# Kernel tuning notes

Hardware: AMD Instinct MI355X
Metric: run time of the kernel (lower is better)

The kernel has to match this reference:

```python
import jax, jax.numpy as jnp
import numpy as np

B, H, W, C = 32, 64, 64, 256


def setup_inputs() -> dict:
    key = jax.random.key(0)
    kq, kk, kv = jax.random.split(key, 3)
    query = jax.random.normal(kq, (B, H, W, C), dtype=jnp.float32)
    keys = jax.random.normal(kk, (B, H, W, C), dtype=jnp.float32)
    values = jax.random.normal(kv, (B, H, W, C), dtype=jnp.float32)
    return {"query": query, "keys": keys, "values": values}


def reference(query, keys, values):
    # A[b,q,k] = sum_{h,w} query[b,h,w,q] * keys[b,h,w,k]
    scores = jnp.einsum("bhwq,bhwk->bqk", query, keys)
    attn = jax.nn.softmax(scores, axis=-1)  # softmax over keys axis
    # out[b,q,h,w] = sum_k attn[b,q,k] * values[b,h,w,k]
    out = jnp.einsum("bqk,bhwk->bqhw", attn, values)
    return out
```

## Files before the change

### kernel.cpp

```cpp
#include <hip/hip_runtime.h>
#include <hip/hip_bf16.h>

#define B_  32
#define HW_ 4096
#define C_  256
#define S_LDS 40

using bf16x8 = __attribute__((ext_vector_type(8))) short;
using f32x4  = __attribute__((ext_vector_type(4))) float;

__device__ __forceinline__ ushort f2bf_rn(float x) {
    uint u = __builtin_bit_cast(uint, x);
    u += 0x7FFFu + ((u >> 16) & 1u);
    return (ushort)(u >> 16);
}
__device__ __forceinline__ uint pk_bf2(float a, float b) {
    return ((uint)f2bf_rn(b) << 16) | (uint)f2bf_rn(a);
}
__device__ __forceinline__ uint pk_rtz(float x0, float x1) {
    return __builtin_amdgcn_perm(__builtin_bit_cast(uint, x1),
                                 __builtin_bit_cast(uint, x0), 0x07060302u);
}
__device__ __forceinline__ void split2_rtz(float x0, float x1, uint& hi2, uint& lo2) {
    uint u0 = __builtin_bit_cast(uint, x0), u1 = __builtin_bit_cast(uint, x1);
    hi2 = __builtin_amdgcn_perm(u1, u0, 0x07060302u);
    float h0 = __builtin_bit_cast(float, u0 & 0xFFFF0000u);
    float h1 = __builtin_bit_cast(float, u1 & 0xFFFF0000u);
    lo2 = pk_rtz(x0 - h0, x1 - h1);
}

__global__ __launch_bounds__(256) void scores_kernel(const float* __restrict__ qg,
                                                     const float* __restrict__ kg,
                                                     float* __restrict__ scores) {
    int x  = blockIdx.x;
    int s  = x & 3;
    int tn = (x >> 2) & 3;
    int tm = (x >> 4) & 1;
    int b  = x >> 5;

    __shared__ __align__(16) ushort Qhi[128 * S_LDS], Qlo[128 * S_LDS];
    __shared__ __align__(16) ushort Khi[64 * S_LDS],  Klo[64 * S_LDS];

    int tid = threadIdx.x, lane = tid & 63, w = tid >> 6;
    int m0 = (w >> 1) * 64;
    int n0 = (w & 1) * 32;
    int g = lane >> 4, r16 = lane & 15;

    int cq = tid & 127;
    int hq = (tid >> 7) * 16;
    int ck = tid & 63;
    int hk = (tid >> 6) * 8;

    const float* qcol = qg + (size_t)b * HW_ * C_ + tm * 128 + cq;
    const float* kcol = kg + (size_t)b * HW_ * C_ + tn * 64 + ck;

    f32x4 acc[4][2];
#pragma unroll
    for (int i = 0; i < 4; ++i)
#pragma unroll
        for (int j = 0; j < 2; ++j) acc[i][j] = (f32x4){0.f, 0.f, 0.f, 0.f};

#define LOAD_QK(qr, kr, itv) {                                                 \
        int hw0 = s * 1024 + (itv) * 32;                                       \
        const float* qp = qcol + (size_t)(hw0 + hq) * C_;                      \
        _Pragma("unroll")                                                      \
        for (int j = 0; j < 16; ++j) qr[j] = qp[(size_t)j * C_];               \
        const float* kp = kcol + (size_t)(hw0 + hk) * C_;                      \
        _Pragma("unroll")                                                      \
        for (int j = 0; j < 8; ++j) kr[j] = kp[(size_t)j * C_];                \
    }

#define CONVERT_STORE(qr, kr) {                                                \
        uint qh[8], ql[8];                                                     \
        _Pragma("unroll")                                                      \
        for (int p = 0; p < 8; ++p) split2_rtz(qr[2*p], qr[2*p+1], qh[p], ql[p]); \
        int qb_ = cq * S_LDS + hq;                                             \
        *reinterpret_cast<uint4*>(&Qhi[qb_])     = make_uint4(qh[0], qh[1], qh[2], qh[3]); \
        *reinterpret_cast<uint4*>(&Qhi[qb_ + 8]) = make_uint4(qh[4], qh[5], qh[6], qh[7]); \
        *reinterpret_cast<uint4*>(&Qlo[qb_])     = make_uint4(ql[0], ql[1], ql[2], ql[3]); \
        *reinterpret_cast<uint4*>(&Qlo[qb_ + 8]) = make_uint4(ql[4], ql[5], ql[6], ql[7]); \
        uint kh[4], kl[4];                                                     \
        _Pragma("unroll")                                                      \
        for (int p = 0; p < 4; ++p) split2_rtz(kr[2*p], kr[2*p+1], kh[p], kl[p]); \
        int kb_ = ck * S_LDS + hk;                                             \
        *reinterpret_cast<uint4*>(&Khi[kb_]) = make_uint4(kh[0], kh[1], kh[2], kh[3]); \
        *reinterpret_cast<uint4*>(&Klo[kb_]) = make_uint4(kl[0], kl[1], kl[2], kl[3]); \
    }

#define MFMA_PHASE() {                                                         \
        bf16x8 ahi[4], alo[4];                                                 \
        _Pragma("unroll")                                                      \
        for (int mi = 0; mi < 4; ++mi) {                                       \
            int off = (m0 + mi * 16 + r16) * S_LDS + g * 8;                    \
            ahi[mi] = *reinterpret_cast<const bf16x8*>(&Qhi[off]);             \
            alo[mi] = *reinterpret_cast<const bf16x8*>(&Qlo[off]);             \
        }                                                                      \
        _Pragma("unroll")                                                      \
        for (int ni = 0; ni < 2; ++ni) {                                       \
            int off = (n0 + ni * 16 + r16) * S_LDS + g * 8;                    \
            bf16x8 bhi = *reinterpret_cast<const bf16x8*>(&Khi[off]);          \
            bf16x8 blo = *reinterpret_cast<const bf16x8*>(&Klo[off]);          \
            _Pragma("unroll")                                                  \
            for (int mi = 0; mi < 4; ++mi) {                                   \
                acc[mi][ni] = __builtin_amdgcn_mfma_f32_16x16x32_bf16(ahi[mi], bhi, acc[mi][ni], 0, 0, 0); \
                acc[mi][ni] = __builtin_amdgcn_mfma_f32_16x16x32_bf16(ahi[mi], blo, acc[mi][ni], 0, 0, 0); \
                acc[mi][ni] = __builtin_amdgcn_mfma_f32_16x16x32_bf16(alo[mi], bhi, acc[mi][ni], 0, 0, 0); \
            }                                                                  \
        }                                                                      \
    }

#define STEP(qc, kc, qn, kn, itv, doload) {                                    \
        if (doload) LOAD_QK(qn, kn, (itv) + 1);                                \
        __syncthreads();                                                       \
        CONVERT_STORE(qc, kc);                                                 \
        __syncthreads();                                                       \
        MFMA_PHASE();                                                          \
    }

    float qa[16], ka[8], qb[16], kb[8];
    LOAD_QK(qa, ka, 0);
    for (int p = 0; p < 16; ++p) {
        STEP(qa, ka, qb, kb, 2 * p, true);
        STEP(qb, kb, qa, ka, 2 * p + 1, p < 15);
    }

#pragma unroll
    for (int mi = 0; mi < 4; ++mi)
#pragma unroll
        for (int ni = 0; ni < 2; ++ni)
#pragma unroll
            for (int r = 0; r < 4; ++r) {
                int qrow = tm * 128 + m0 + mi * 16 + g * 4 + r;
                int kc   = tn * 64 + n0 + ni * 16 + r16;
                atomicAdd(&scores[((size_t)b * 256 + qrow) * 256 + kc], acc[mi][ni][r]);
            }
#undef STEP
#undef MFMA_PHASE
#undef CONVERT_STORE
#undef LOAD_QK
}

__global__ __launch_bounds__(256) void softmax_kernel(const float* __restrict__ scores,
                                                      ushort* __restrict__ attn) {
    int wid  = blockIdx.x * 4 + (threadIdx.x >> 6);
    int lane = threadIdx.x & 63;
    const float4 v = *reinterpret_cast<const float4*>(scores + (size_t)wid * 256 + lane * 4);
    float m = fmaxf(fmaxf(v.x, v.y), fmaxf(v.z, v.w));
#pragma unroll
    for (int off = 32; off; off >>= 1) m = fmaxf(m, __shfl_xor(m, off, 64));
    float e0 = __expf(v.x - m), e1 = __expf(v.y - m), e2 = __expf(v.z - m), e3 = __expf(v.w - m);
    float ssum = e0 + e1 + e2 + e3;
#pragma unroll
    for (int off = 32; off; off >>= 1) ssum += __shfl_xor(ssum, off, 64);
    float inv = 1.0f / ssum;
    uint2 o;
    o.x = pk_bf2(e0 * inv, e1 * inv);
    o.y = pk_bf2(e2 * inv, e3 * inv);
    *reinterpret_cast<uint2*>(attn + (size_t)wid * 256 + lane * 4) = o;
}

__global__ __launch_bounds__(256) void pv_kernel(const ushort* __restrict__ attn,
                                                 const float* __restrict__ vg,
                                                 float* __restrict__ out) {
    int b   = blockIdx.x >> 6;
    int hw0 = (blockIdx.x & 63) * 64;
    int tid = threadIdx.x, lane = tid & 63, w = tid >> 6;
    int m0  = w * 64;
    int g   = lane >> 4, r16 = lane & 15;

    f32x4 acc[4][4];
#pragma unroll
    for (int i = 0; i < 4; ++i)
#pragma unroll
        for (int j = 0; j < 4; ++j) acc[i][j] = (f32x4){0.f, 0.f, 0.f, 0.f};

    for (int ks = 0; ks < 8; ++ks) {
        int k0 = ks * 32;
        bf16x8 a[4];
#pragma unroll
        for (int mi = 0; mi < 4; ++mi) {
            int qrow = m0 + mi * 16 + r16;
            a[mi] = *reinterpret_cast<const bf16x8*>(attn + ((size_t)b * 256 + qrow) * 256 + k0 + g * 8);
        }
        float4 vv[4][2];
#pragma unroll
        for (int ni = 0; ni < 4; ++ni) {
            int hw = hw0 + ni * 16 + r16;
            const float* vp = vg + ((size_t)(b * HW_ + hw)) * C_ + k0 + g * 8;
            vv[ni][0] = *reinterpret_cast<const float4*>(vp);
            vv[ni][1] = *reinterpret_cast<const float4*>(vp + 4);
        }
#pragma unroll
        for (int ni = 0; ni < 4; ++ni) {
            bf16x8 bf;
            uint* bu = reinterpret_cast<uint*>(&bf);
            bu[0] = pk_rtz(vv[ni][0].x, vv[ni][0].y);
            bu[1] = pk_rtz(vv[ni][0].z, vv[ni][0].w);
            bu[2] = pk_rtz(vv[ni][1].x, vv[ni][1].y);
            bu[3] = pk_rtz(vv[ni][1].z, vv[ni][1].w);
#pragma unroll
            for (int mi = 0; mi < 4; ++mi)
                acc[mi][ni] = __builtin_amdgcn_mfma_f32_16x16x32_bf16(a[mi], bf, acc[mi][ni], 0, 0, 0);
        }
    }

#pragma unroll
    for (int mi = 0; mi < 4; ++mi)
#pragma unroll
        for (int ni = 0; ni < 4; ++ni)
#pragma unroll
            for (int r = 0; r < 4; ++r) {
                int qrow = m0 + mi * 16 + g * 4 + r;
                int hw   = hw0 + ni * 16 + r16;
                out[((size_t)b * 256 + qrow) * 4096 + hw] = acc[mi][ni][r];
            }
}

extern "C" void kernel_launch(void* const* d_in, const int* in_sizes, int n_in,
                              void* d_out, int out_size, void* d_ws, size_t ws_size,
                              hipStream_t stream) {
    const float* q = (const float*)d_in[0];
    const float* k = (const float*)d_in[1];
    const float* v = (const float*)d_in[2];
    float* out = (float*)d_out;

    float*  scores = (float*)d_ws;
    ushort* attn   = (ushort*)((char*)d_ws + (size_t)B_ * 256 * 256 * 4);

    (void)hipMemsetAsync(d_ws, 0, (size_t)B_ * 256 * 256 * 4, stream);
    scores_kernel<<<1024, 256, 0, stream>>>(q, k, scores);
    softmax_kernel<<<2048, 256, 0, stream>>>(scores, attn);
    pv_kernel<<<2048, 256, 0, stream>>>(attn, v, out);
}
```

Baseline: 215.3 us.

## Enlarge scores tile to 128x128 per block and double-buffer PV loads

```diff
diff --git a/kernel.cpp b/kernel.cpp
--- a/kernel.cpp
+++ b/kernel.cpp
@@ -29,30 +29,28 @@
     lo2 = pk_rtz(x0 - h0, x1 - h1);
 }
 
-__global__ __launch_bounds__(256) void scores_kernel(const float* __restrict__ qg,
-                                                     const float* __restrict__ kg,
-                                                     float* __restrict__ scores) {
+__global__ __launch_bounds__(512, 4) void scores_kernel(const float* __restrict__ qg,
+                                                        const float* __restrict__ kg,
+                                                        float* __restrict__ scores) {
     int x  = blockIdx.x;
     int s  = x & 3;
-    int tn = (x >> 2) & 3;
-    int tm = (x >> 4) & 1;
-    int b  = x >> 5;
+    int tn = (x >> 2) & 1;
+    int tm = (x >> 3) & 1;
+    int b  = x >> 4;
 
     __shared__ __align__(16) ushort Qhi[128 * S_LDS], Qlo[128 * S_LDS];
-    __shared__ __align__(16) ushort Khi[64 * S_LDS],  Klo[64 * S_LDS];
+    __shared__ __align__(16) ushort Khi[128 * S_LDS], Klo[128 * S_LDS];
 
     int tid = threadIdx.x, lane = tid & 63, w = tid >> 6;
-    int m0 = (w >> 1) * 64;
-    int n0 = (w & 1) * 32;
+    int m0 = (w >> 2) * 64;
+    int n0 = (w & 3) * 32;
     int g = lane >> 4, r16 = lane & 15;
 
-    int cq = tid & 127;
-    int hq = (tid >> 7) * 16;
-    int ck = tid & 63;
-    int hk = (tid >> 6) * 8;
-
-    const float* qcol = qg + (size_t)b * HW_ * C_ + tm * 128 + cq;
-    const float* kcol = kg + (size_t)b * HW_ * C_ + tn * 64 + ck;
+    int cc = tid & 127;
+    int hh = (tid >> 7) * 8;
+
+    const float* qcol = qg + (size_t)b * HW_ * C_ + tm * 128 + cc;
+    const float* kcol = kg + (size_t)b * HW_ * C_ + tn * 128 + cc;
 
     f32x4 acc[4][2];
 #pragma unroll
@@ -61,30 +59,27 @@
         for (int j = 0; j < 2; ++j) acc[i][j] = (f32x4){0.f, 0.f, 0.f, 0.f};
 
 #define LOAD_QK(qr, kr, itv) {                                                 \
-        int hw0 = s * 1024 + (itv) * 32;                                       \
-        const float* qp = qcol + (size_t)(hw0 + hq) * C_;                      \
-        _Pragma("unroll")                                                      \
-        for (int j = 0; j < 16; ++j) qr[j] = qp[(size_t)j * C_];               \
-        const float* kp = kcol + (size_t)(hw0 + hk) * C_;                      \
+        int hw0 = s * 1024 + (itv) * 32 + hh;                                  \
+        const float* qp = qcol + (size_t)hw0 * C_;                             \
+        const float* kp = kcol + (size_t)hw0 * C_;                             \
+        _Pragma("unroll")                                                      \
+        for (int j = 0; j < 8; ++j) qr[j] = qp[(size_t)j * C_];                \
         _Pragma("unroll")                                                      \
         for (int j = 0; j < 8; ++j) kr[j] = kp[(size_t)j * C_];                \
     }
 
 #define CONVERT_STORE(qr, kr) {                                                \
-        uint qh[8], ql[8];                                                     \
-        _Pragma("unroll")                                                      \
-        for (int p = 0; p < 8; ++p) split2_rtz(qr[2*p], qr[2*p+1], qh[p], ql[p]); \
-        int qb_ = cq * S_LDS + hq;                                             \
-        *reinterpret_cast<uint4*>(&Qhi[qb_])     = make_uint4(qh[0], qh[1], qh[2], qh[3]); \
-        *reinterpret_cast<uint4*>(&Qhi[qb_ + 8]) = make_uint4(qh[4], qh[5], qh[6], qh[7]); \
-        *reinterpret_cast<uint4*>(&Qlo[qb_])     = make_uint4(ql[0], ql[1], ql[2], ql[3]); \
-        *reinterpret_cast<uint4*>(&Qlo[qb_ + 8]) = make_uint4(ql[4], ql[5], ql[6], ql[7]); \
-        uint kh[4], kl[4];                                                     \
-        _Pragma("unroll")                                                      \
-        for (int p = 0; p < 4; ++p) split2_rtz(kr[2*p], kr[2*p+1], kh[p], kl[p]); \
-        int kb_ = ck * S_LDS + hk;                                             \
-        *reinterpret_cast<uint4*>(&Khi[kb_]) = make_uint4(kh[0], kh[1], kh[2], kh[3]); \
-        *reinterpret_cast<uint4*>(&Klo[kb_]) = make_uint4(kl[0], kl[1], kl[2], kl[3]); \
+        uint qh[4], ql[4], kh[4], kl[4];                                       \
+        _Pragma("unroll")                                                      \
+        for (int p = 0; p < 4; ++p) {                                          \
+            split2_rtz(qr[2*p], qr[2*p+1], qh[p], ql[p]);                      \
+            split2_rtz(kr[2*p], kr[2*p+1], kh[p], kl[p]);                      \
+        }                                                                      \
+        int base_ = cc * S_LDS + hh;                                           \
+        *reinterpret_cast<uint4*>(&Qhi[base_]) = make_uint4(qh[0], qh[1], qh[2], qh[3]); \
+        *reinterpret_cast<uint4*>(&Qlo[base_]) = make_uint4(ql[0], ql[1], ql[2], ql[3]); \
+        *reinterpret_cast<uint4*>(&Khi[base_]) = make_uint4(kh[0], kh[1], kh[2], kh[3]); \
+        *reinterpret_cast<uint4*>(&Klo[base_]) = make_uint4(kl[0], kl[1], kl[2], kl[3]); \
     }
 
 #define MFMA_PHASE() {                                                         \
@@ -117,7 +112,7 @@
         MFMA_PHASE();                                                          \
     }
 
-    float qa[16], ka[8], qb[16], kb[8];
+    float qa[8], ka[8], qb[8], kb[8];
     LOAD_QK(qa, ka, 0);
     for (int p = 0; p < 16; ++p) {
         STEP(qa, ka, qb, kb, 2 * p, true);
@@ -131,7 +126,7 @@
 #pragma unroll
             for (int r = 0; r < 4; ++r) {
                 int qrow = tm * 128 + m0 + mi * 16 + g * 4 + r;
-                int kc   = tn * 64 + n0 + ni * 16 + r16;
+                int kc   = tn * 128 + n0 + ni * 16 + r16;
                 atomicAdd(&scores[((size_t)b * 256 + qrow) * 256 + kc], acc[mi][ni][r]);
             }
 #undef STEP
@@ -159,50 +154,64 @@
     *reinterpret_cast<uint2*>(attn + (size_t)wid * 256 + lane * 4) = o;
 }
 
-__global__ __launch_bounds__(256) void pv_kernel(const ushort* __restrict__ attn,
-                                                 const float* __restrict__ vg,
-                                                 float* __restrict__ out) {
+__global__ __launch_bounds__(256, 3) void pv_kernel(const ushort* __restrict__ attn,
+                                                    const float* __restrict__ vg,
+                                                    float* __restrict__ out) {
     int b   = blockIdx.x >> 6;
     int hw0 = (blockIdx.x & 63) * 64;
     int tid = threadIdx.x, lane = tid & 63, w = tid >> 6;
     int m0  = w * 64;
     int g   = lane >> 4, r16 = lane & 15;
 
+    const ushort* abase = attn + (size_t)b * 256 * 256 + g * 8;
+    const float*  vbase = vg + ((size_t)(b * HW_ + hw0 + r16)) * C_ + g * 8;
+
     f32x4 acc[4][4];
 #pragma unroll
     for (int i = 0; i < 4; ++i)
 #pragma unroll
         for (int j = 0; j < 4; ++j) acc[i][j] = (f32x4){0.f, 0.f, 0.f, 0.f};
 
-    for (int ks = 0; ks < 8; ++ks) {
-        int k0 = ks * 32;
-        bf16x8 a[4];
-#pragma unroll
-        for (int mi = 0; mi < 4; ++mi) {
-            int qrow = m0 + mi * 16 + r16;
-            a[mi] = *reinterpret_cast<const bf16x8*>(attn + ((size_t)b * 256 + qrow) * 256 + k0 + g * 8);
-        }
-        float4 vv[4][2];
-#pragma unroll
-        for (int ni = 0; ni < 4; ++ni) {
-            int hw = hw0 + ni * 16 + r16;
-            const float* vp = vg + ((size_t)(b * HW_ + hw)) * C_ + k0 + g * 8;
-            vv[ni][0] = *reinterpret_cast<const float4*>(vp);
-            vv[ni][1] = *reinterpret_cast<const float4*>(vp + 4);
-        }
-#pragma unroll
-        for (int ni = 0; ni < 4; ++ni) {
-            bf16x8 bf;
-            uint* bu = reinterpret_cast<uint*>(&bf);
-            bu[0] = pk_rtz(vv[ni][0].x, vv[ni][0].y);
-            bu[1] = pk_rtz(vv[ni][0].z, vv[ni][0].w);
-            bu[2] = pk_rtz(vv[ni][1].x, vv[ni][1].y);
-            bu[3] = pk_rtz(vv[ni][1].z, vv[ni][1].w);
-#pragma unroll
-            for (int mi = 0; mi < 4; ++mi)
-                acc[mi][ni] = __builtin_amdgcn_mfma_f32_16x16x32_bf16(a[mi], bf, acc[mi][ni], 0, 0, 0);
-        }
-    }
+#define K3_LOAD(abuf, vbuf, ksv) {                                             \
+        int k0_ = (ksv) * 32;                                                  \
+        _Pragma("unroll")                                                      \
+        for (int mi = 0; mi < 4; ++mi)                                         \
+            abuf[mi] = *reinterpret_cast<const bf16x8*>(abase + (size_t)(m0 + mi * 16 + r16) * 256 + k0_); \
+        _Pragma("unroll")                                                      \
+        for (int ni = 0; ni < 4; ++ni) {                                       \
+            const float* vp_ = vbase + (size_t)ni * 16 * C_ + k0_;             \
+            vbuf[ni][0] = *reinterpret_cast<const float4*>(vp_);               \
+            vbuf[ni][1] = *reinterpret_cast<const float4*>(vp_ + 4);           \
+        }                                                                      \
+    }
+
+#define K3_COMPUTE(abuf, vbuf) {                                               \
+        _Pragma("unroll")                                                      \
+        for (int ni = 0; ni < 4; ++ni) {                                       \
+            bf16x8 bf;                                                         \
+            uint* bu = reinterpret_cast<uint*>(&bf);                           \
+            bu[0] = pk_rtz(vbuf[ni][0].x, vbuf[ni][0].y);                      \
+            bu[1] = pk_rtz(vbuf[ni][0].z, vbuf[ni][0].w);                      \
+            bu[2] = pk_rtz(vbuf[ni][1].x, vbuf[ni][1].y);                      \
+            bu[3] = pk_rtz(vbuf[ni][1].z, vbuf[ni][1].w);                      \
+            _Pragma("unroll")                                                  \
+            for (int mi = 0; mi < 4; ++mi)                                     \
+                acc[mi][ni] = __builtin_amdgcn_mfma_f32_16x16x32_bf16(abuf[mi], bf, acc[mi][ni], 0, 0, 0); \
+        }                                                                      \
+    }
+
+    bf16x8 aA[4], aB[4];
+    float4 vA[4][2], vB[4][2];
+    K3_LOAD(aA, vA, 0);
+#pragma unroll
+    for (int p = 0; p < 4; ++p) {
+        K3_LOAD(aB, vB, 2 * p + 1);
+        K3_COMPUTE(aA, vA);
+        if (p < 3) K3_LOAD(aA, vA, 2 * p + 2);
+        K3_COMPUTE(aB, vB);
+    }
+#undef K3_LOAD
+#undef K3_COMPUTE
 
 #pragma unroll
     for (int mi = 0; mi < 4; ++mi)
@@ -228,7 +237,7 @@
     ushort* attn   = (ushort*)((char*)d_ws + (size_t)B_ * 256 * 256 * 4);
 
     (void)hipMemsetAsync(d_ws, 0, (size_t)B_ * 256 * 256 * 4, stream);
-    scores_kernel<<<1024, 256, 0, stream>>>(q, k, scores);
+    scores_kernel<<<512, 512, 0, stream>>>(q, k, scores);
     softmax_kernel<<<2048, 256, 0, stream>>>(scores, attn);
     pv_kernel<<<2048, 256, 0, stream>>>(attn, v, out);
 }
```

Result: no change. 215.4 us (+0.1%).
